# Kernel tuning notes

Hardware: AMD Instinct MI355X
Metric: run time of the kernel (lower is better)

## Reference

```python
import jax, jax.numpy as jnp
import numpy as np

HEADS = 16
DIM_HEAD = 64
SCALE = DIM_HEAD ** -0.5


def setup_inputs() -> dict:
    key = jax.random.key(0)
    k1, k2, k3, k4 = jax.random.split(key, 4)
    b, n, dim = 2, 2048, 1024
    inner = HEADS * DIM_HEAD  # 1024
    x = jax.random.normal(k1, (b, n, dim), dtype=jnp.float32)
    mask = jax.random.randint(k2, (b, n), 0, 2, dtype=jnp.int32)
    Wqkv = jax.random.normal(k3, (dim, inner), dtype=jnp.float32) * (dim ** -0.5)
    Wout = jax.random.normal(k4, (inner, dim), dtype=jnp.float32) * (inner ** -0.5)
    bout = jnp.zeros((dim,), dtype=jnp.float32)
    return {"x": x, "mask": mask, "Wqkv": Wqkv, "Wout": Wout, "bout": bout}


def reference(x, mask, Wqkv, Wout, bout):
    b, n, _ = x.shape
    # shared projection: w acts as q = k = v (CRATE subspace attention)
    w = jnp.einsum('bnd,de->bne', x, Wqkv)
    w = w.reshape(b, n, HEADS, DIM_HEAD).transpose(0, 2, 1, 3)  # b h n d
    dots = jnp.einsum('bhid,bhjd->bhij', w, w) * SCALE           # b h n n
    attn = jax.nn.softmax(dots, axis=-1)
    # post-softmax multiplicative masking (mask=1 zeros the column)
    m = mask[:, None, None, :].astype(attn.dtype)
    attn = attn * (1.0 - m)
    out = jnp.einsum('bhij,bhjd->bhid', attn, w)                 # b h n d
    out = out.transpose(0, 2, 1, 3).reshape(b, n, HEADS * DIM_HEAD)
    return jnp.einsum('bne,ed->bnd', out, Wout) + bout
```

## Files before the change

### kernel.cpp

```cpp
#include <hip/hip_runtime.h>
#include <hip/hip_bf16.h>
#include <stdint.h>

typedef unsigned short u16;
typedef unsigned int u32;
typedef __bf16 bf16x8 __attribute__((ext_vector_type(8)));
typedef float f32x4 __attribute__((ext_vector_type(4)));
typedef float f32x16 __attribute__((ext_vector_type(16)));
typedef u32 u32x4 __attribute__((ext_vector_type(4)));

#define AS1 __attribute__((address_space(1)))
#define AS3 __attribute__((address_space(3)))

__device__ __forceinline__ void async16(const u16* g, u16* l) {
  __builtin_amdgcn_global_load_lds((const AS1 uint32_t*)(const void*)g,
                                   (AS3 uint32_t*)l, 16, 0, 0);
}

__device__ __forceinline__ u16 f2bf(float v) {
  union { __hip_bfloat16 b; u16 u; } c; c.b = __float2bfloat16(v); return c.u;
}

__device__ __forceinline__ u32 pkbf(float a, float b) {
  return (u32)f2bf(a) | ((u32)f2bf(b) << 16);
}

__device__ __forceinline__ void swap32(u32 &a, u32 &b) {
  asm("v_permlane32_swap_b32 %0, %1" : "+v"(a), "+v"(b));
}

__device__ __forceinline__ uint4 pack8(float4 lo, float4 hi) {
  uint4 q;
  q.x = (u32)f2bf(lo.x) | ((u32)f2bf(lo.y) << 16);
  q.y = (u32)f2bf(lo.z) | ((u32)f2bf(lo.w) << 16);
  q.z = (u32)f2bf(hi.x) | ((u32)f2bf(hi.y) << 16);
  q.w = (u32)f2bf(hi.z) | ((u32)f2bf(hi.w) << 16);
  return q;
}

__global__ void cvt_x(const float* __restrict__ in, u16* __restrict__ out) {
  int i = (blockIdx.x * 256 + threadIdx.x) * 8;
  float4 lo = *(const float4*)(in + i);
  float4 hi = *(const float4*)(in + i + 4);
  *(uint4*)(out + i) = pack8(lo, hi);
}

__global__ void transpose1024_cvt2(const float* __restrict__ in0, u16* __restrict__ out0,
                                   const float* __restrict__ in1, u16* __restrict__ out1) {
  const float* in = blockIdx.z ? in1 : in0;
  u16* out = blockIdx.z ? out1 : out0;
  __shared__ u16 tile[32][33];
  int tx = threadIdx.x, ty = threadIdx.y;
  int c0 = blockIdx.x * 32, r0 = blockIdx.y * 32;
#pragma unroll
  for (int i = 0; i < 32; i += 8)
    tile[ty + i][tx] = f2bf(in[(size_t)(r0 + ty + i) * 1024 + c0 + tx]);
  __syncthreads();
#pragma unroll
  for (int i = 0; i < 32; i += 8)
    out[(size_t)(c0 + ty + i) * 1024 + r0 + tx] = tile[tx][ty + i];
}

__global__ void scale_transpose_v(const u16* __restrict__ w, const int* __restrict__ mask,
                                  u16* __restrict__ Vt) {
  __shared__ u16 tile[32][33];
  const int tx = threadIdx.x, ty = threadIdx.y;
  const int j0 = blockIdx.x * 32, d0 = blockIdx.y * 32;
  const int bh = blockIdx.z, b = bh >> 4, hc = (bh & 15) * 64;
#pragma unroll
  for (int i = 0; i < 32; i += 8) {
    int j = j0 + ty + i;
    u16 v = w[(size_t)(b * 2048 + j) * 1024 + hc + d0 + tx];
    tile[ty + i][tx] = mask[b * 2048 + j] ? (u16)0 : v;
  }
  __syncthreads();
#pragma unroll
  for (int i = 0; i < 32; i += 8)
    Vt[((size_t)bh * 64 + d0 + ty + i) * 2048 + j0 + tx] = tile[tx][ty + i];
}

template<bool OUT_F32>
__launch_bounds__(256)
__global__ void gemm_bt(const u16* __restrict__ A, const u16* __restrict__ BT,
                        void* __restrict__ Cp, const float* __restrict__ bias,
                        int M, int N, int K) {
  __shared__ __align__(16) u16 As[2][128 * 32];
  __shared__ __align__(16) u16 Bs[2][64 * 32];
  const int t = threadIdx.x;
  const int lane = t & 63, wave = t >> 6;
  const int m0 = blockIdx.x * 128, n0 = blockIdx.y * 64;
  const int wm = (wave & 1) * 64, wn = (wave >> 1) * 32;
  const int lrow = lane & 15, quad = lane >> 4;

  f32x4 acc[4][2] = {};

  const int ar = t >> 2, ac = (t & 3) * 8;
  const u16* gA = A + (size_t)(m0 + ar) * K + ac;
  const u16* gB = BT + (size_t)(n0 + ar) * K + ac;

  for (int k0 = 0; k0 < K; k0 += 64) {
    async16(gA + k0,                       &As[0][t * 8]);
    async16(gA + k0 + (size_t)64 * K,      &As[0][t * 8 + 2048]);
    async16(gA + k0 + 32,                  &As[1][t * 8]);
    async16(gA + k0 + 32 + (size_t)64 * K, &As[1][t * 8 + 2048]);
    async16(gB + k0,                       &Bs[0][t * 8]);
    async16(gB + k0 + 32,                  &Bs[1][t * 8]);
    __syncthreads();

#pragma unroll
    for (int kk = 0; kk < 2; kk++) {
      bf16x8 af[4], bfr[2];
#pragma unroll
      for (int i = 0; i < 4; i++)
        af[i] = *(const bf16x8*)&As[kk][(wm + i * 16 + lrow) * 32 + quad * 8];
#pragma unroll
      for (int j = 0; j < 2; j++)
        bfr[j] = *(const bf16x8*)&Bs[kk][(wn + j * 16 + lrow) * 32 + quad * 8];
#pragma unroll
      for (int i = 0; i < 4; i++)
#pragma unroll
        for (int j = 0; j < 2; j++)
          acc[i][j] = __builtin_amdgcn_mfma_f32_16x16x32_bf16(af[i], bfr[j], acc[i][j], 0, 0, 0);
    }
    __syncthreads();
  }

  float bv[2];
#pragma unroll
  for (int j = 0; j < 2; j++)
    bv[j] = bias ? bias[n0 + wn + j * 16 + lrow] : 0.f;

#pragma unroll
  for (int i = 0; i < 4; i++) {
#pragma unroll
    for (int r = 0; r < 4; r++) {
      int row = m0 + wm + i * 16 + quad * 4 + r;
#pragma unroll
      for (int j = 0; j < 2; j++) {
        size_t ci = (size_t)row * N + n0 + wn + j * 16 + lrow;
        float v = acc[i][j][r] + bv[j];
        if (OUT_F32) ((float*)Cp)[ci] = v;
        else ((u16*)Cp)[ci] = f2bf(v);
      }
    }
  }
}

#define C1 0.18033688f
#define C2 -28.853901f
__launch_bounds__(256)
__global__ void attn_kernel(const u16* __restrict__ w, const u16* __restrict__ Vt,
                            u16* __restrict__ y) {
  __shared__ __align__(16) u16 Ws[2][64 * 64];
  __shared__ __align__(16) u16 VTs[2][64 * 64];
  const int t = threadIdx.x, lane = t & 63, wv = t >> 6;
  const int ql = lane & 31, hi = lane >> 5, swz = ql & 7;
  const int bh = blockIdx.y, b = bh >> 4, hc = (bh & 15) * 64;
  const int q0 = blockIdx.x * 128;
  const size_t rowb = (size_t)b * 2048;

  const int skey = t >> 3;
  const int scl = ((t & 7) ^ (skey & 7)) * 8;
  const u16* kg = w + rowb * 1024 + hc;
  const u16* vg = Vt + (size_t)bh * 64 * 2048;

  bf16x8 qf[4];
  {
    const size_t qrow = rowb + q0 + wv * 32 + ql;
#pragma unroll
    for (int ks = 0; ks < 4; ks++)
      qf[ks] = *(const bf16x8*)&w[qrow * 1024 + hc + ks * 16 + hi * 8];
  }

  f32x16 o0 = {}, o1 = {};
  float lrun = 0.f;

#define STAGE(buf, j0s) do { \
    async16(kg + (size_t)((j0s) + skey) * 1024 + scl,       &Ws[buf][t * 8]); \
    async16(kg + (size_t)((j0s) + skey + 32) * 1024 + scl,  &Ws[buf][2048 + t * 8]); \
    async16(vg + (size_t)skey * 2048 + (j0s) + scl,         &VTs[buf][t * 8]); \
    async16(vg + (size_t)(skey + 32) * 2048 + (j0s) + scl,  &VTs[buf][2048 + t * 8]); \
  } while (0)

  STAGE(0, 0);
  __syncthreads();

  int cur = 0;
  for (int j0 = 0; j0 < 2048; j0 += 64) {
    if (j0 + 64 < 2048) STAGE(cur ^ 1, j0 + 64);

    u32x4 pa[4];
#pragma unroll
    for (int g = 0; g < 2; g++) {
      f32x16 p = {};
#pragma unroll
      for (int ks = 0; ks < 4; ks++) {
        bf16x8 af = *(const bf16x8*)
            &Ws[cur][(g * 32 + ql) * 64 + (((ks * 2 + hi) ^ swz) * 8)];
        p = __builtin_amdgcn_mfma_f32_32x32x16_bf16(af, qf[ks], p, 0, 0, 0);
      }
      float e[16];
#pragma unroll
      for (int r = 0; r < 16; r++) {
        e[r] = exp2f(fmaf(p[r], C1, C2));
        lrun += e[r];
      }
      u32 a0 = pkbf(e[0], e[1]),   b0 = pkbf(e[4], e[5]);   swap32(a0, b0);
      u32 a1 = pkbf(e[2], e[3]),   b1 = pkbf(e[6], e[7]);   swap32(a1, b1);
      u32 a2 = pkbf(e[8], e[9]),   b2 = pkbf(e[12], e[13]); swap32(a2, b2);
      u32 a3 = pkbf(e[10], e[11]), b3 = pkbf(e[14], e[15]); swap32(a3, b3);
      u32x4 f0 = {a0, a1, b0, b1};
      u32x4 f1 = {a2, a3, b2, b3};
      pa[2 * g + 0] = f0;
      pa[2 * g + 1] = f1;
    }

    __builtin_amdgcn_s_setprio(1);
#pragma unroll
    for (int ks = 0; ks < 4; ks++) {
      union { u32x4 u; bf16x8 bf; } cv; cv.u = pa[ks];
      bf16x8 vb0 = *(const bf16x8*)
          &VTs[cur][ql * 64 + (((ks * 2 + hi) ^ swz) * 8)];
      bf16x8 vb1 = *(const bf16x8*)
          &VTs[cur][(32 + ql) * 64 + (((ks * 2 + hi) ^ swz) * 8)];
      o0 = __builtin_amdgcn_mfma_f32_32x32x16_bf16(cv.bf, vb0, o0, 0, 0, 0);
      o1 = __builtin_amdgcn_mfma_f32_32x32x16_bf16(cv.bf, vb1, o1, 0, 0, 0);
    }
    __builtin_amdgcn_s_setprio(0);

    __syncthreads();
    cur ^= 1;
  }
#undef STAGE

  lrun += __shfl_xor(lrun, 32, 64);
  const float inv = 1.f / lrun;
#pragma unroll
  for (int r = 0; r < 16; r++) {
    const int qo = (r & 3) + 8 * (r >> 2) + 4 * hi;
    const float iv = __int_as_float(
        __builtin_amdgcn_ds_bpermute(qo * 4, __float_as_int(inv)));
    const size_t orow = rowb + q0 + wv * 32 + qo;
    y[orow * 1024 + hc + ql]      = f2bf(o0[r] * iv);
    y[orow * 1024 + hc + 32 + ql] = f2bf(o1[r] * iv);
  }
}

extern "C" void kernel_launch(void* const* d_in, const int* in_sizes, int n_in,
                              void* d_out, int out_size, void* d_ws, size_t ws_size,
                              hipStream_t stream) {
  const float* x    = (const float*)d_in[0];
  const int* mask   = (const int*)d_in[1];
  const float* Wqkv = (const float*)d_in[2];
  const float* Wout = (const float*)d_in[3];
  const float* bout = (const float*)d_in[4];
  float* out = (float*)d_out;

  u16* w     = (u16*)d_ws;
  u16* y     = w + 4096 * 1024;
  u16* WqkvT = y + 4096 * 1024;
  u16* WoutT = WqkvT + 1024 * 1024;
  u16* Vt    = WoutT + 1024 * 1024;
  u16* xb    = y;

  cvt_x<<<2048, 256, 0, stream>>>(x, xb);
  transpose1024_cvt2<<<dim3(32, 32, 2), dim3(32, 8), 0, stream>>>(Wqkv, WqkvT, Wout, WoutT);
  gemm_bt<false><<<dim3(32, 16), 256, 0, stream>>>(xb, WqkvT, w, nullptr, 4096, 1024, 1024);
  scale_transpose_v<<<dim3(64, 2, 32), dim3(32, 8), 0, stream>>>(w, mask, Vt);
  attn_kernel<<<dim3(16, 32), 256, 0, stream>>>(w, Vt, y);
  gemm_bt<true><<<dim3(32, 16), 256, 0, stream>>>(y, WoutT, out, bout, 4096, 1024, 1024);
}
```

Measured before the change: 194.1 us.

## Split attention key range across two wave groups and merge partial outputs

The attention kernel now launches 512 threads per block. Two groups of four waves each process half of the 2048 keys into separate shared-memory buffers, then the partial outputs and row sums are combined through shared memory before normalisation. The goal is more waves per CU and shorter per-wave serial loops, which helps because the grid of 512 blocks only lightly fills the GPU. The cost is double the LDS footprint, a merge step with extra shared traffic and a barrier. The bf16 pair packing also switches to a single v_cvt_pk_bf16_f32 instruction in place of two scalar conversions.

Measured after the change: 174.7 us. -10.0%, faster.

```diff
diff --git a/kernel.cpp b/kernel.cpp
--- a/kernel.cpp
+++ b/kernel.cpp
@@ -22,7 +22,9 @@
 }
 
 __device__ __forceinline__ u32 pkbf(float a, float b) {
-  return (u32)f2bf(a) | ((u32)f2bf(b) << 16);
+  u32 r;
+  asm("v_cvt_pk_bf16_f32 %0, %1, %2" : "=v"(r) : "v"(a), "v"(b));
+  return r;
 }
 
 __device__ __forceinline__ void swap32(u32 &a, u32 &b) {
@@ -148,25 +150,28 @@
 
 #define C1 0.18033688f
 #define C2 -28.853901f
-__launch_bounds__(256)
+__launch_bounds__(512)
 __global__ void attn_kernel(const u16* __restrict__ w, const u16* __restrict__ Vt,
                             u16* __restrict__ y) {
-  __shared__ __align__(16) u16 Ws[2][64 * 64];
-  __shared__ __align__(16) u16 VTs[2][64 * 64];
+  __shared__ __align__(16) u16 smem[2][2][2][64 * 64];
   const int t = threadIdx.x, lane = t & 63, wv = t >> 6;
+  const int qg = wv & 3, kgr = wv >> 2;
   const int ql = lane & 31, hi = lane >> 5, swz = ql & 7;
   const int bh = blockIdx.y, b = bh >> 4, hc = (bh & 15) * 64;
   const int q0 = blockIdx.x * 128;
   const size_t rowb = (size_t)b * 2048;
 
-  const int skey = t >> 3;
-  const int scl = ((t & 7) ^ (skey & 7)) * 8;
-  const u16* kg = w + rowb * 1024 + hc;
-  const u16* vg = Vt + (size_t)bh * 64 * 2048;
+  const int tt = t & 255;
+  const int sg = t >> 8;
+  const int skey = tt >> 3;
+  const int scl = ((tt & 7) ^ (skey & 7)) * 8;
+  const int sjb = sg * 1024;
+  const u16* kptr = w + rowb * 1024 + hc;
+  const u16* vptr = Vt + (size_t)bh * 64 * 2048;
 
   bf16x8 qf[4];
   {
-    const size_t qrow = rowb + q0 + wv * 32 + ql;
+    const size_t qrow = rowb + q0 + qg * 32 + ql;
 #pragma unroll
     for (int ks = 0; ks < 4; ks++)
       qf[ks] = *(const bf16x8*)&w[qrow * 1024 + hc + ks * 16 + hi * 8];
@@ -176,18 +181,21 @@
   float lrun = 0.f;
 
 #define STAGE(buf, j0s) do { \
-    async16(kg + (size_t)((j0s) + skey) * 1024 + scl,       &Ws[buf][t * 8]); \
-    async16(kg + (size_t)((j0s) + skey + 32) * 1024 + scl,  &Ws[buf][2048 + t * 8]); \
-    async16(vg + (size_t)skey * 2048 + (j0s) + scl,         &VTs[buf][t * 8]); \
-    async16(vg + (size_t)(skey + 32) * 2048 + (j0s) + scl,  &VTs[buf][2048 + t * 8]); \
+    async16(kptr + (size_t)(sjb + (j0s) + skey) * 1024 + scl,       &smem[0][sg][buf][tt * 8]); \
+    async16(kptr + (size_t)(sjb + (j0s) + skey + 32) * 1024 + scl,  &smem[0][sg][buf][2048 + tt * 8]); \
+    async16(vptr + (size_t)skey * 2048 + sjb + (j0s) + scl,         &smem[1][sg][buf][tt * 8]); \
+    async16(vptr + (size_t)(skey + 32) * 2048 + sjb + (j0s) + scl,  &smem[1][sg][buf][2048 + tt * 8]); \
   } while (0)
 
   STAGE(0, 0);
   __syncthreads();
 
   int cur = 0;
-  for (int j0 = 0; j0 < 2048; j0 += 64) {
-    if (j0 + 64 < 2048) STAGE(cur ^ 1, j0 + 64);
+  for (int j0 = 0; j0 < 1024; j0 += 64) {
+    if (j0 + 64 < 1024) STAGE(cur ^ 1, j0 + 64);
+
+    const u16* Wt = smem[0][kgr][cur];
+    const u16* Vts = smem[1][kgr][cur];
 
     u32x4 pa[4];
 #pragma unroll
@@ -196,7 +204,7 @@
 #pragma unroll
       for (int ks = 0; ks < 4; ks++) {
         bf16x8 af = *(const bf16x8*)
-            &Ws[cur][(g * 32 + ql) * 64 + (((ks * 2 + hi) ^ swz) * 8)];
+            &Wt[(g * 32 + ql) * 64 + (((ks * 2 + hi) ^ swz) * 8)];
         p = __builtin_amdgcn_mfma_f32_32x32x16_bf16(af, qf[ks], p, 0, 0, 0);
       }
       float e[16];
@@ -220,9 +228,9 @@
     for (int ks = 0; ks < 4; ks++) {
       union { u32x4 u; bf16x8 bf; } cv; cv.u = pa[ks];
       bf16x8 vb0 = *(const bf16x8*)
-          &VTs[cur][ql * 64 + (((ks * 2 + hi) ^ swz) * 8)];
+          &Vts[ql * 64 + (((ks * 2 + hi) ^ swz) * 8)];
       bf16x8 vb1 = *(const bf16x8*)
-          &VTs[cur][(32 + ql) * 64 + (((ks * 2 + hi) ^ swz) * 8)];
+          &Vts[(32 + ql) * 64 + (((ks * 2 + hi) ^ swz) * 8)];
       o0 = __builtin_amdgcn_mfma_f32_32x32x16_bf16(cv.bf, vb0, o0, 0, 0, 0);
       o1 = __builtin_amdgcn_mfma_f32_32x32x16_bf16(cv.bf, vb1, o1, 0, 0, 0);
     }
@@ -234,15 +242,30 @@
 #undef STAGE
 
   lrun += __shfl_xor(lrun, 32, 64);
-  const float inv = 1.f / lrun;
-#pragma unroll
-  for (int r = 0; r < 16; r++) {
-    const int qo = (r & 3) + 8 * (r >> 2) + 4 * hi;
-    const float iv = __int_as_float(
-        __builtin_amdgcn_ds_bpermute(qo * 4, __float_as_int(inv)));
-    const size_t orow = rowb + q0 + wv * 32 + qo;
-    y[orow * 1024 + hc + ql]      = f2bf(o0[r] * iv);
-    y[orow * 1024 + hc + 32 + ql] = f2bf(o1[r] * iv);
+
+  float* mrg = (float*)smem;
+  float* slot = mrg + (qg * 64 + lane) * 33;
+  if (kgr == 1) {
+#pragma unroll
+    for (int r = 0; r < 16; r++) { slot[r] = o0[r]; slot[16 + r] = o1[r]; }
+    slot[32] = lrun;
+  }
+  __syncthreads();
+  if (kgr == 0) {
+#pragma unroll
+    for (int r = 0; r < 16; r++) { o0[r] += slot[r]; o1[r] += slot[16 + r]; }
+    lrun += slot[32];
+
+    const float inv = 1.f / lrun;
+#pragma unroll
+    for (int r = 0; r < 16; r++) {
+      const int qo = (r & 3) + 8 * (r >> 2) + 4 * hi;
+      const float iv = __int_as_float(
+          __builtin_amdgcn_ds_bpermute(qo * 4, __float_as_int(inv)));
+      const size_t orow = rowb + q0 + qg * 32 + qo;
+      y[orow * 1024 + hc + ql]      = f2bf(o0[r] * iv);
+      y[orow * 1024 + hc + 32 + ql] = f2bf(o1[r] * iv);
+    }
   }
 }
 
@@ -267,6 +290,6 @@
   transpose1024_cvt2<<<dim3(32, 32, 2), dim3(32, 8), 0, stream>>>(Wqkv, WqkvT, Wout, WoutT);
   gemm_bt<false><<<dim3(32, 16), 256, 0, stream>>>(xb, WqkvT, w, nullptr, 4096, 1024, 1024);
   scale_transpose_v<<<dim3(64, 2, 32), dim3(32, 8), 0, stream>>>(w, mask, Vt);
-  attn_kernel<<<dim3(16, 32), 256, 0, stream>>>(w, Vt, y);
+  attn_kernel<<<dim3(16, 32), 512, 0, stream>>>(w, Vt, y);
   gemm_bt<true><<<dim3(32, 16), 256, 0, stream>>>(y, WoutT, out, bout, 4096, 1024, 1024);
 }
```
